# Kernel optimization log

Hardware: AMD Instinct MI355X
Metric: run time of the kernel (lower is better)

## Reference

```python
import jax, jax.numpy as jnp
import numpy as np

ELEM, EMBD = 512, 512

def setup_inputs() -> dict:
    key = jax.random.key(0)
    ks = jax.random.split(key, 7)
    s = 1.0 / np.sqrt(ELEM)
    return {
        "x": jax.random.normal(ks[0], (8, 2048, ELEM), dtype=jnp.float32),
        "Wq": jax.random.normal(ks[1], (ELEM, EMBD), dtype=jnp.float32) * s,
        "bq": jnp.zeros((EMBD,), dtype=jnp.float32),
        "Wk": jax.random.normal(ks[2], (ELEM, EMBD), dtype=jnp.float32) * s,
        "bk": jnp.zeros((EMBD,), dtype=jnp.float32),
        "Wv": jax.random.normal(ks[3], (ELEM, EMBD), dtype=jnp.float32) * s,
        "bv": jnp.zeros((EMBD,), dtype=jnp.float32),
    }

def reference(x, Wq, bq, Wk, bk, Wv, bv):
    # x: [N, S, E]
    q = x @ Wq + bq            # [N, S, D]
    k = x @ Wk + bk            # [N, S, D]
    v = x @ Wv + bv            # [N, S, D]
    # NOTE: original has no 1/sqrt(d) scaling.
    logits = jnp.einsum('nsd,ntd->nst', q, k)   # [N, S, S]
    attn = jax.nn.softmax(logits, axis=-1)
    return jnp.einsum('nst,ntd->nsd', attn, v)  # [N, S, D]
```

## Files before the change

kernel.cpp:

```cpp
#include <hip/hip_runtime.h>
#include <hip/hip_fp16.h>

#define SEQ 2048
#define DIM 512

typedef __attribute__((ext_vector_type(8))) short short8;
typedef __attribute__((ext_vector_type(4))) float f32x4;
typedef _Float16 h8 __attribute__((ext_vector_type(8)));
typedef _Float16 h4 __attribute__((ext_vector_type(4)));

#define MFMA16(a, b, c) __builtin_amdgcn_mfma_f32_16x16x32_f16((a), (b), (c), 0, 0, 0)

#define GLOAD_LDS16(g, l)                                                              \
    __builtin_amdgcn_global_load_lds(                                                  \
        (const __attribute__((address_space(1))) unsigned int*)(g),                    \
        (__attribute__((address_space(3))) unsigned int*)(l), 16, 0, 0)

template <int MODE>
__global__ __launch_bounds__(512, 1) void gemmc(
    const _Float16* __restrict__ A, const _Float16* __restrict__ B,
    const float* __restrict__ bq, const float* __restrict__ bk,
    const float* __restrict__ bv,
    _Float16* __restrict__ oq, _Float16* __restrict__ ok, _Float16* __restrict__ ovt,
    float* __restrict__ of, int bat0) {
    extern __shared__ char sm[];
    constexpr int T  = (MODE == 0) ? 16 : (MODE == 1) ? 8 : 32;
    constexpr int PA = (MODE == 0) ? 512 : (MODE == 1) ? 512 : 4096;
    constexpr int PB = (MODE == 0) ? 1024 : (MODE == 1) ? 512 : 2048;

    int tid = threadIdx.x, wid = tid >> 6, lane = tid & 63, r = lane & 15, g = lane >> 4;
    int wm = wid >> 1, wn = wid & 1;
    int m0 = blockIdx.x * 256, n0 = blockIdx.y * 128, bz = blockIdx.z;

    const _Float16 *Ab, *Bb;
    if (MODE == 0) {
        Ab = A + (size_t)m0 * 512;
        Bb = B + (size_t)n0 * 1024;
    } else if (MODE == 1) {
        int b = bat0 + bz;
        Ab = A + ((size_t)(b * SEQ) + m0) * 512;
        Bb = B + ((size_t)(b * SEQ) + n0) * 512;
    } else {
        int b = bat0 + bz;
        Ab = A + (size_t)bz * (SEQ * 4096) + (size_t)m0 * 4096;
        Bb = B + (size_t)b * (512 * SEQ) + (size_t)n0 * 2048;
    }

    const char* gA[4];
    const char* gB[2];
    int ldsA[4], ldsB[2];
#pragma unroll
    for (int j = 0; j < 4; ++j) {
        int ci = j * 512 + tid;
        int row = ci >> 3, cl = ci & 7;
        int col16 = cl ^ (row & 7);
        gA[j] = (const char*)Ab + (size_t)row * (PA * 2) + col16 * 16;
        ldsA[j] = ci * 16;
    }
#pragma unroll
    for (int j = 0; j < 2; ++j) {
        int ci = j * 512 + tid;
        int row = ci >> 3, cl = ci & 7;
        int col16 = cl ^ (row & 7);
        gB[j] = (const char*)Bb + (size_t)row * (PB * 2) + col16 * 16;
        ldsB[j] = ci * 16;
    }
    int offA[4][2], offB[4][2];
#pragma unroll
    for (int m = 0; m < 4; ++m) {
        int rowA = wm * 64 + m * 16 + r;
        int rowB = wn * 64 + m * 16 + r;
#pragma unroll
        for (int ks = 0; ks < 2; ++ks) {
            offA[m][ks] = rowA * 128 + (((ks * 4 + g) ^ (rowA & 7)) * 16);
            offB[m][ks] = rowB * 128 + (((ks * 4 + g) ^ (rowB & 7)) * 16);
        }
    }

    f32x4 acc[4][4];
#pragma unroll
    for (int m = 0; m < 4; ++m)
#pragma unroll
        for (int n = 0; n < 4; ++n) acc[m][n] = (f32x4)(0.0f);

    auto STG = [&](int t, int b) {
        int ka = (MODE == 0) ? ((t & 7) * 128) : (t * 128);
        int kb = t * 128;
        char* dA = sm + b * 49152;
        char* dB = sm + b * 49152 + 32768;
#pragma unroll
        for (int j = 0; j < 4; ++j) GLOAD_LDS16(gA[j] + ka, dA + ldsA[j]);
#pragma unroll
        for (int j = 0; j < 2; ++j) GLOAD_LDS16(gB[j] + kb, dB + ldsB[j]);
    };

    STG(0, 0);
    STG(1, 1);
    asm volatile("s_waitcnt vmcnt(6)" ::: "memory");
    __builtin_amdgcn_s_barrier();

#pragma unroll
    for (int t = 0; t < T; ++t) {
        const int buf = t % 3;
        if (t + 2 < T) STG(t + 2, (t + 2) % 3);
        const char* bA = sm + buf * 49152;
        const char* bB = sm + buf * 49152 + 32768;
        h8 af[4][2], bf[4][2];
#pragma unroll
        for (int m = 0; m < 4; ++m)
#pragma unroll
            for (int ks = 0; ks < 2; ++ks) {
                af[m][ks] = *(const h8*)(bA + offA[m][ks]);
                bf[m][ks] = *(const h8*)(bB + offB[m][ks]);
            }
        __builtin_amdgcn_s_setprio(1);
#pragma unroll
        for (int ks = 0; ks < 2; ++ks)
#pragma unroll
            for (int m = 0; m < 4; ++m)
#pragma unroll
                for (int n = 0; n < 4; ++n)
                    acc[m][n] = MFMA16(af[m][ks], bf[n][ks], acc[m][n]);
        __builtin_amdgcn_s_setprio(0);
        if (t + 2 < T) asm volatile("s_waitcnt vmcnt(6)" ::: "memory");
        else if (t + 1 < T) asm volatile("s_waitcnt vmcnt(0)" ::: "memory");
        if (t + 1 < T) __builtin_amdgcn_s_barrier();
    }

    if (MODE == 0) {
        int p = n0 >> 9;
        int ncl = n0 & 511;
        const float* bias = (p == 0) ? bq : (p == 1) ? bk : bv;
#pragma unroll
        for (int n = 0; n < 4; ++n) {
            int col = ncl + wn * 64 + n * 16 + r;
            float bi = bias[col];
#pragma unroll
            for (int m = 0; m < 4; ++m) {
                int grow0 = m0 + wm * 64 + m * 16 + 4 * g;
                if (p == 0) {
                    for (int reg = 0; reg < 4; ++reg)
                        oq[(size_t)(grow0 + reg) * 512 + col] =
                            (_Float16)(acc[m][n][reg] + bi);
                } else if (p == 1) {
                    for (int reg = 0; reg < 4; ++reg)
                        ok[(size_t)(grow0 + reg) * 512 + col] =
                            (_Float16)(acc[m][n][reg] + bi);
                } else {
                    int b = grow0 >> 11, s0 = grow0 & 2047;
                    h4 pv;
                    pv[0] = (_Float16)(acc[m][n][0] + bi);
                    pv[1] = (_Float16)(acc[m][n][1] + bi);
                    pv[2] = (_Float16)(acc[m][n][2] + bi);
                    pv[3] = (_Float16)(acc[m][n][3] + bi);
                    *(h4*)(&ovt[(size_t)b * (512 * 2048) + (size_t)col * 2048 + s0]) = pv;
                }
            }
        }
    } else if (MODE == 1) {
        float* sb = of + (size_t)bz * (SEQ * (size_t)SEQ);
#pragma unroll
        for (int n = 0; n < 4; ++n) {
            int col = n0 + wn * 64 + n * 16 + r;
#pragma unroll
            for (int m = 0; m < 4; ++m) {
                int grow0 = m0 + wm * 64 + m * 16 + 4 * g;
                for (int reg = 0; reg < 4; ++reg)
                    sb[(size_t)(grow0 + reg) * SEQ + col] = acc[m][n][reg];
            }
        }
    } else {
        int b = bat0 + bz;
#pragma unroll
        for (int n = 0; n < 4; ++n) {
            int col = n0 + wn * 64 + n * 16 + r;
#pragma unroll
            for (int m = 0; m < 4; ++m) {
                int grow0 = m0 + wm * 64 + m * 16 + 4 * g;
                for (int reg = 0; reg < 4; ++reg)
                    of[(size_t)(b * SEQ + grow0 + reg) * 512 + col] = acc[m][n][reg];
            }
        }
    }
}

__global__ __launch_bounds__(256) void k0a_splitw(
    const float* __restrict__ Wq, const float* __restrict__ Wk, const float* __restrict__ Wv,
    _Float16* __restrict__ wstk) {
    int idx = blockIdx.x * 256 + threadIdx.x;
    int p = idx >> 18;
    int rem = idx & 262143;
    int k = rem >> 9, n = rem & 511;
    const float* W = (p == 0) ? Wq : (p == 1) ? Wk : Wv;
    float w = W[rem];
    _Float16 h = (_Float16)w;
    size_t base = (size_t)(p * 512 + n) * 1024;
    wstk[base + k] = h;
    wstk[base + 512 + k] = (_Float16)(w - (float)h);
}

__global__ __launch_bounds__(256) void k0b_splitx(
    const float* __restrict__ x, _Float16* __restrict__ xh) {
    size_t i = (size_t)(blockIdx.x * 256 + threadIdx.x) * 4;
    float4 v = *(const float4*)(x + i);
    h4 h;
    h[0] = (_Float16)v.x; h[1] = (_Float16)v.y;
    h[2] = (_Float16)v.z; h[3] = (_Float16)v.w;
    *(h4*)(xh + i) = h;
}

__global__ __launch_bounds__(256) void k3_softmax(float* __restrict__ sbuf) {
    size_t row = blockIdx.x;
    float* srow = sbuf + row * SEQ;
    int tid = threadIdx.x, lane = tid & 63, wid = tid >> 6;
    float4 v0 = *(const float4*)(srow + tid * 8);
    float4 v1 = *(const float4*)(srow + tid * 8 + 4);
    float m = fmaxf(fmaxf(fmaxf(v0.x, v0.y), fmaxf(v0.z, v0.w)),
                    fmaxf(fmaxf(v1.x, v1.y), fmaxf(v1.z, v1.w)));
    for (int d = 1; d < 64; d <<= 1) m = fmaxf(m, __shfl_xor(m, d));
    __shared__ float red1[4], red2[4];
    if (lane == 0) red1[wid] = m;
    __syncthreads();
    m = fmaxf(fmaxf(red1[0], red1[1]), fmaxf(red1[2], red1[3]));
    float e[8];
    e[0] = __expf(v0.x - m); e[1] = __expf(v0.y - m);
    e[2] = __expf(v0.z - m); e[3] = __expf(v0.w - m);
    e[4] = __expf(v1.x - m); e[5] = __expf(v1.y - m);
    e[6] = __expf(v1.z - m); e[7] = __expf(v1.w - m);
    float s = ((e[0] + e[1]) + (e[2] + e[3])) + ((e[4] + e[5]) + (e[6] + e[7]));
    for (int d = 1; d < 64; d <<= 1) s += __shfl_xor(s, d);
    if (lane == 0) red2[wid] = s;
    __syncthreads();
    s = (red2[0] + red2[1]) + (red2[2] + red2[3]);
    float inv = 1.0f / s;
    h8 ph;
    for (int j = 0; j < 8; ++j) ph[j] = (_Float16)(e[j] * inv);
    *(h8*)((char*)srow + (size_t)tid * 16) = ph;
}

extern "C" void kernel_launch(void* const* d_in, const int* in_sizes, int n_in,
                              void* d_out, int out_size, void* d_ws, size_t ws_size,
                              hipStream_t stream) {
    const float* x  = (const float*)d_in[0];
    const float* Wq = (const float*)d_in[1];
    const float* bq = (const float*)d_in[2];
    const float* Wk = (const float*)d_in[3];
    const float* bk = (const float*)d_in[4];
    const float* Wv = (const float*)d_in[5];
    const float* bv = (const float*)d_in[6];
    float* out = (float*)d_out;

    char* ws = (char*)d_ws;
    const size_t QSZ = 16777216;
    _Float16* wstk = (_Float16*)(ws);
    _Float16* xh = (_Float16*)(ws + 3145728);
    _Float16* qh = (_Float16*)(ws + 3145728 + 1 * QSZ);
    _Float16* kh = (_Float16*)(ws + 3145728 + 2 * QSZ);
    _Float16* vt = (_Float16*)(ws + 3145728 + 3 * QSZ);
    const size_t sbase = 3145728 + 4 * QSZ;

    const int LDSB = 3 * 49152;
    hipFuncSetAttribute((const void*)gemmc<0>,
                        hipFuncAttributeMaxDynamicSharedMemorySize, LDSB);
    hipFuncSetAttribute((const void*)gemmc<1>,
                        hipFuncAttributeMaxDynamicSharedMemorySize, LDSB);
    hipFuncSetAttribute((const void*)gemmc<2>,
                        hipFuncAttributeMaxDynamicSharedMemorySize, LDSB);

    k0a_splitw<<<3072, 256, 0, stream>>>(Wq, Wk, Wv, wstk);
    k0b_splitx<<<8192, 256, 0, stream>>>(x, xh);
    gemmc<0><<<dim3(64, 12), 512, LDSB, stream>>>(xh, wstk, bq, bk, bv,
                                                  qh, kh, vt, nullptr, 0);

    size_t avail = (ws_size > sbase) ? (ws_size - sbase) : 0;
    int chunk = (int)(avail / QSZ);
    if (chunk < 1) chunk = 1;
    if (chunk > 8) chunk = 8;
    float* sc = (float*)(ws + sbase);
    for (int b0 = 0; b0 < 8; b0 += chunk) {
        int nb = (8 - b0 < chunk) ? (8 - b0) : chunk;
        gemmc<1><<<dim3(8, 16, nb), 512, LDSB, stream>>>(qh, kh, nullptr, nullptr, nullptr,
                                                         nullptr, nullptr, nullptr, sc, b0);
        k3_softmax<<<dim3(nb * SEQ), 256, 0, stream>>>(sc);
        gemmc<2><<<dim3(8, 4, nb), 512, LDSB, stream>>>((const _Float16*)sc, vt,
                                                        nullptr, nullptr, nullptr,
                                                        nullptr, nullptr, nullptr, out, b0);
    }
}
```

Baseline: 189.9 us.

## Halve K-tile depth to shrink LDS footprint and raise block occupancy

Reduces the per-stage K tile from 64 to 32 halfs, halving LDS per block to allow multiple resident blocks per CU, and raises the launch bounds minimum-blocks hint. The loop now runs twice as many pipeline stages with one MFMA k-step each. It aims to hide latency through more concurrent blocks, but adds twice the barriers and waitcnts per unit of work. The tighter register cap and narrower 4-way swizzle risk spills or LDS bank conflicts.

```diff
diff --git a/kernel.cpp b/kernel.cpp
--- a/kernel.cpp
+++ b/kernel.cpp
@@ -17,14 +17,14 @@
         (__attribute__((address_space(3))) unsigned int*)(l), 16, 0, 0)
 
 template <int MODE>
-__global__ __launch_bounds__(512, 1) void gemmc(
+__global__ __launch_bounds__(512, 4) void gemmc(
     const _Float16* __restrict__ A, const _Float16* __restrict__ B,
     const float* __restrict__ bq, const float* __restrict__ bk,
     const float* __restrict__ bv,
     _Float16* __restrict__ oq, _Float16* __restrict__ ok, _Float16* __restrict__ ovt,
     float* __restrict__ of, int bat0) {
     extern __shared__ char sm[];
-    constexpr int T  = (MODE == 0) ? 16 : (MODE == 1) ? 8 : 32;
+    constexpr int T  = (MODE == 0) ? 32 : (MODE == 1) ? 16 : 64;
     constexpr int PA = (MODE == 0) ? 512 : (MODE == 1) ? 512 : 4096;
     constexpr int PB = (MODE == 0) ? 1024 : (MODE == 1) ? 512 : 2048;
 
@@ -46,35 +46,31 @@
         Bb = B + (size_t)b * (512 * SEQ) + (size_t)n0 * 2048;
     }
 
-    const char* gA[4];
-    const char* gB[2];
-    int ldsA[4], ldsB[2];
-#pragma unroll
-    for (int j = 0; j < 4; ++j) {
+    const char* gA[2];
+    const char* gB;
+    int ldsA[2], ldsB;
+#pragma unroll
+    for (int j = 0; j < 2; ++j) {
         int ci = j * 512 + tid;
-        int row = ci >> 3, cl = ci & 7;
-        int col16 = cl ^ (row & 7);
+        int row = ci >> 2, cl = ci & 3;
+        int col16 = cl ^ (row & 3);
         gA[j] = (const char*)Ab + (size_t)row * (PA * 2) + col16 * 16;
         ldsA[j] = ci * 16;
     }
-#pragma unroll
-    for (int j = 0; j < 2; ++j) {
-        int ci = j * 512 + tid;
-        int row = ci >> 3, cl = ci & 7;
-        int col16 = cl ^ (row & 7);
-        gB[j] = (const char*)Bb + (size_t)row * (PB * 2) + col16 * 16;
-        ldsB[j] = ci * 16;
-    }
-    int offA[4][2], offB[4][2];
+    {
+        int ci = tid;
+        int row = ci >> 2, cl = ci & 3;
+        int col16 = cl ^ (row & 3);
+        gB = (const char*)Bb + (size_t)row * (PB * 2) + col16 * 16;
+        ldsB = ci * 16;
+    }
+    int offA[4], offB[4];
 #pragma unroll
     for (int m = 0; m < 4; ++m) {
         int rowA = wm * 64 + m * 16 + r;
         int rowB = wn * 64 + m * 16 + r;
-#pragma unroll
-        for (int ks = 0; ks < 2; ++ks) {
-            offA[m][ks] = rowA * 128 + (((ks * 4 + g) ^ (rowA & 7)) * 16);
-            offB[m][ks] = rowB * 128 + (((ks * 4 + g) ^ (rowB & 7)) * 16);
-        }
+        offA[m] = rowA * 64 + ((g ^ (rowA & 3)) * 16);
+        offB[m] = rowB * 64 + ((g ^ (rowB & 3)) * 16);
     }
 
     f32x4 acc[4][4];
@@ -84,45 +80,40 @@
         for (int n = 0; n < 4; ++n) acc[m][n] = (f32x4)(0.0f);
 
     auto STG = [&](int t, int b) {
-        int ka = (MODE == 0) ? ((t & 7) * 128) : (t * 128);
-        int kb = t * 128;
-        char* dA = sm + b * 49152;
-        char* dB = sm + b * 49152 + 32768;
-#pragma unroll
-        for (int j = 0; j < 4; ++j) GLOAD_LDS16(gA[j] + ka, dA + ldsA[j]);
-#pragma unroll
-        for (int j = 0; j < 2; ++j) GLOAD_LDS16(gB[j] + kb, dB + ldsB[j]);
+        int ka = (MODE == 0) ? ((t & 15) * 64) : (t * 64);
+        int kb = t * 64;
+        char* dA = sm + b * 24576;
+        char* dB = sm + b * 24576 + 16384;
+        GLOAD_LDS16(gA[0] + ka, dA + ldsA[0]);
+        GLOAD_LDS16(gA[1] + ka, dA + ldsA[1]);
+        GLOAD_LDS16(gB + kb, dB + ldsB);
     };
 
     STG(0, 0);
     STG(1, 1);
-    asm volatile("s_waitcnt vmcnt(6)" ::: "memory");
+    asm volatile("s_waitcnt vmcnt(3)" ::: "memory");
     __builtin_amdgcn_s_barrier();
 
 #pragma unroll
     for (int t = 0; t < T; ++t) {
         const int buf = t % 3;
         if (t + 2 < T) STG(t + 2, (t + 2) % 3);
-        const char* bA = sm + buf * 49152;
-        const char* bB = sm + buf * 49152 + 32768;
-        h8 af[4][2], bf[4][2];
+        const char* bA = sm + buf * 24576;
+        const char* bB = sm + buf * 24576 + 16384;
+        h8 af[4], bf[4];
+#pragma unroll
+        for (int m = 0; m < 4; ++m) {
+            af[m] = *(const h8*)(bA + offA[m]);
+            bf[m] = *(const h8*)(bB + offB[m]);
+        }
+        __builtin_amdgcn_s_setprio(1);
 #pragma unroll
         for (int m = 0; m < 4; ++m)
 #pragma unroll
-            for (int ks = 0; ks < 2; ++ks) {
-                af[m][ks] = *(const h8*)(bA + offA[m][ks]);
-                bf[m][ks] = *(const h8*)(bB + offB[m][ks]);
-            }
-        __builtin_amdgcn_s_setprio(1);
-#pragma unroll
-        for (int ks = 0; ks < 2; ++ks)
-#pragma unroll
-            for (int m = 0; m < 4; ++m)
-#pragma unroll
-                for (int n = 0; n < 4; ++n)
-                    acc[m][n] = MFMA16(af[m][ks], bf[n][ks], acc[m][n]);
+            for (int n = 0; n < 4; ++n)
+                acc[m][n] = MFMA16(af[m], bf[n], acc[m][n]);
         __builtin_amdgcn_s_setprio(0);
-        if (t + 2 < T) asm volatile("s_waitcnt vmcnt(6)" ::: "memory");
+        if (t + 2 < T) asm volatile("s_waitcnt vmcnt(3)" ::: "memory");
         else if (t + 1 < T) asm volatile("s_waitcnt vmcnt(0)" ::: "memory");
         if (t + 1 < T) __builtin_amdgcn_s_barrier();
     }
@@ -259,7 +250,7 @@
     _Float16* vt = (_Float16*)(ws + 3145728 + 3 * QSZ);
     const size_t sbase = 3145728 + 4 * QSZ;
 
-    const int LDSB = 3 * 49152;
+    const int LDSB = 3 * 24576;
     hipFuncSetAttribute((const void*)gemmc<0>,
                         hipFuncAttributeMaxDynamicSharedMemorySize, LDSB);
     hipFuncSetAttribute((const void*)gemmc<1>,
```

New measurement: 216.7 us. +14.1%, slower.
